# Optimization experiments

Measured on AMD Instinct MI355X. Metric: run time of the kernel, lower is better.

The kernel has to match this reference:

```python
import jax, jax.numpy as jnp
import numpy as np

S, B, D = 2048, 2, 768
H = 12
R = 64  # adapter bottleneck


def setup_inputs() -> dict:
    key = jax.random.key(0)
    ks = jax.random.split(key, 16)
    d = {
        'query': jax.random.normal(ks[0], (S, B, D), jnp.float32),
        'key':   jax.random.normal(ks[1], (S, B, D), jnp.float32),
        'value': jax.random.normal(ks[2], (S, B, D), jnp.float32),
        'in_proj_w': jax.random.normal(ks[3], (3 * D, D), jnp.float32) * (D ** -0.5),
        'in_proj_b': jax.random.normal(ks[4], (3 * D,), jnp.float32) * 0.02,
        'ssf_scale_1': 1.0 + 0.02 * jax.random.normal(ks[5], (3 * D,), jnp.float32),
        'ssf_shift_1': 0.02 * jax.random.normal(ks[6], (3 * D,), jnp.float32),
        'lora1_down_w': jax.random.normal(ks[7], (R, D), jnp.float32) * (D ** -0.5),
        'lora1_down_b': jnp.zeros((R,), jnp.float32),
        'lora1_up_w': jax.random.normal(ks[8], (3 * D, R), jnp.float32) * 0.02,
        'lora1_up_b': jnp.zeros((3 * D,), jnp.float32),
        'lora1_scale': jnp.ones((1,), jnp.float32),
        'out_w': jax.random.normal(ks[9], (D, D), jnp.float32) * (D ** -0.5),
        'out_b': jnp.zeros((D,), jnp.float32),
        'ssf_scale_2': 1.0 + 0.02 * jax.random.normal(ks[10], (D,), jnp.float32),
        'ssf_shift_2': 0.02 * jax.random.normal(ks[11], (D,), jnp.float32),
        'lora2_down_w': jax.random.normal(ks[12], (R, D), jnp.float32) * (D ** -0.5),
        'lora2_down_b': jnp.zeros((R,), jnp.float32),
        'lora2_up_w': jax.random.normal(ks[13], (D, R), jnp.float32) * 0.02,
        'lora2_up_b': jnp.zeros((D,), jnp.float32),
        'lora2_scale': jnp.ones((1,), jnp.float32),
        'num_heads': H,
    }
    return d


def _adapter(x, dw, db, uw, ub, scale):
    # down -> relu -> up -> * scalar (dropout inactive, add_residual=False)
    h = jax.nn.relu(jnp.einsum('sbd,rd->sbr', x, dw) + db)
    return (jnp.einsum('sbr,er->sbe', h, uw) + ub) * scale[0]


def reference(query, key, value, in_proj_w, in_proj_b, ssf_scale_1, ssf_shift_1,
              lora1_down_w, lora1_down_b, lora1_up_w, lora1_up_b, lora1_scale,
              out_w, out_b, ssf_scale_2, ssf_shift_2,
              lora2_down_w, lora2_down_b, lora2_up_w, lora2_up_b, lora2_scale,
              num_heads):
    tgt, bsz, d = query.shape
    hd = d // num_heads
    scaling = hd ** -0.5
    # fused QKV projection + SSF scale/shift + LoRA adapter on query
    qkv = jnp.einsum('sbd,ed->sbe', query, in_proj_w) + in_proj_b
    qkv = qkv * ssf_scale_1 + ssf_shift_1
    qkv = qkv + _adapter(query, lora1_down_w, lora1_down_b, lora1_up_w, lora1_up_b, lora1_scale)
    q, k, v = jnp.split(qkv, 3, axis=-1)
    q = q * scaling
    # [S,B,D] -> [B*H, S, hd]
    def to_heads(t):
        return t.reshape(tgt, bsz * num_heads, hd).transpose(1, 0, 2)
    q, k, v = to_heads(q), to_heads(k), to_heads(v)
    attn = jax.nn.softmax(jnp.einsum('nqh,nkh->nqk', q, k), axis=-1)
    out = jnp.einsum('nqk,nkh->nqh', attn, v)  # [B*H, S, hd]
    out = out.transpose(1, 0, 2).reshape(tgt, bsz, d)
    # lora2 on pre-projection attn output
    ad2 = _adapter(out, lora2_down_w, lora2_down_b, lora2_up_w, lora2_up_b, lora2_scale)
    o = jnp.einsum('sbd,ed->sbe', out, out_w) + out_b
    o = o * ssf_scale_2 + ssf_shift_2
    return o + ad2
```

## Files before the change

### kernel.cpp

```cpp
#include <hip/hip_runtime.h>
#include <stdint.h>

typedef float f32x4 __attribute__((ext_vector_type(4)));
typedef _Float16 f16x8 __attribute__((ext_vector_type(8)));
typedef _Float16 f16x4 __attribute__((ext_vector_type(4)));
typedef unsigned int u32x2 __attribute__((ext_vector_type(2)));

#define MFMAH(a, b, c) __builtin_amdgcn_mfma_f32_16x16x32_f16(a, b, c, 0, 0, 0)

#define GLOAD16(gp, lp) __builtin_amdgcn_global_load_lds( \
    (__attribute__((address_space(1))) void*)(void*)(gp), \
    (__attribute__((address_space(3))) void*)(void*)(lp), 16, 0, 0)

#define QSCALE (0.125f * 1.44269504f)
#define SMOFF 8.0f

static __device__ inline f32x4 zero4() { f32x4 z; z[0]=0.f; z[1]=0.f; z[2]=0.f; z[3]=0.f; return z; }

static __device__ inline unsigned int pk2(float a, float b) {
  return __builtin_bit_cast(unsigned int, __builtin_amdgcn_cvt_pkrtz(a, b));
}

__global__ void k_tof16_multi(const float* __restrict__ s0, const float* __restrict__ s1,
                              const float* __restrict__ s2, const float* __restrict__ s3,
                              const float* __restrict__ s4,
                              _Float16* __restrict__ d0, _Float16* __restrict__ d1,
                              _Float16* __restrict__ d2, _Float16* __restrict__ d3,
                              _Float16* __restrict__ d4,
                              int n0, int n1, int n2, int n3, int n4) {
  int total = n0 + n1 + n2 + n3 + n4;
  for (int i = blockIdx.x*blockDim.x + threadIdx.x; i < total; i += gridDim.x*blockDim.x) {
    const float* src; _Float16* dst; int j = i;
    if (j < n0) { src = s0; dst = d0; }
    else { j -= n0;
      if (j < n1) { src = s1; dst = d1; }
      else { j -= n1;
        if (j < n2) { src = s2; dst = d2; }
        else { j -= n2;
          if (j < n3) { src = s3; dst = d3; }
          else { j -= n3; src = s4; dst = d4; }
        }
      }
    }
    float4 v = ((const float4*)src)[j];
    f16x4 o;
    o[0] = (_Float16)v.x; o[1] = (_Float16)v.y; o[2] = (_Float16)v.z; o[3] = (_Float16)v.w;
    ((f16x4*)dst)[j] = o;
  }
}

__global__ void k_prep(const float* __restrict__ uw1, const float* __restrict__ s1,
                       const float* __restrict__ lsc1, _Float16* __restrict__ up1,
                       const float* __restrict__ uw2, const float* __restrict__ s2,
                       const float* __restrict__ lsc2, _Float16* __restrict__ up2,
                       const float* __restrict__ b1, const float* __restrict__ sh1,
                       const float* __restrict__ ub1, float* __restrict__ c1,
                       const float* __restrict__ b2, const float* __restrict__ sh2,
                       const float* __restrict__ ub2, float* __restrict__ c2) {
  int i = blockIdx.x*blockDim.x + threadIdx.x;
  if (i < 2304*64) up1[i] = (_Float16)(uw1[i] * lsc1[0] / s1[i >> 6]);
  if (i < 768*64)  up2[i] = (_Float16)(uw2[i] * lsc2[0] / s2[i >> 6]);
  if (i < 2304)    c1[i] = s1[i]*b1[i] + sh1[i] + lsc1[0]*ub1[i];
  if (i < 768)     c2[i] = s2[i]*b2[i] + sh2[i] + lsc2[0]*ub2[i];
}

__global__ __launch_bounds__(256) void k_lora_h(const _Float16* __restrict__ A,
    const _Float16* __restrict__ Dw, const float* __restrict__ db, _Float16* __restrict__ H) {
  const int wave = threadIdx.x >> 6, lane = threadIdx.x & 63;
  const int g = lane >> 4, li = lane & 15;
  const int rowbase = blockIdx.x * 16;
  f32x4 acc = zero4();
  for (int k0 = 0; k0 < 768; k0 += 32) {
    f16x8 a = *(const f16x8*)(A + (size_t)(rowbase + li)*768 + k0 + g*8);
    f16x8 b = *(const f16x8*)(Dw + (size_t)(wave*16 + li)*768 + k0 + g*8);
    acc = MFMAH(a, b, acc);
  }
  int r = wave*16 + li;
  float bias = db[r];
  #pragma unroll
  for (int j = 0; j < 4; j++) {
    float v = acc[j] + bias;
    H[(size_t)(rowbase + g*4 + j)*64 + r] = (_Float16)fmaxf(v, 0.f);
  }
}

template<int EPI>
__global__ __launch_bounds__(256) void k_gemm(
    const _Float16* __restrict__ A, const _Float16* __restrict__ B,
    const _Float16* __restrict__ Ha, const _Float16* __restrict__ Up,
    const float* __restrict__ Sc, const float* __restrict__ Cst,
    float* __restrict__ Cout, _Float16* __restrict__ qh,
    _Float16* __restrict__ kh, _Float16* __restrict__ vT) {
  __shared__ _Float16 lsA[2][4096];
  __shared__ _Float16 lsB[2][4096];
  const int wave = threadIdx.x >> 6, lane = threadIdx.x & 63;
  const int g = lane >> 4, li = lane & 15;
  const int wr = wave >> 1, wc = wave & 1;
  const int rb = blockIdx.x * 128, cb = blockIdx.y * 128;

  f32x4 acc[4][4];
  #pragma unroll
  for (int m = 0; m < 4; m++)
    #pragma unroll
    for (int n = 0; n < 4; n++) acc[m][n] = zero4();

  auto stage = [&](int buf, int k0) {
    #pragma unroll
    for (int c = 0; c < 2; c++) {
      int p = (wave*2 + c)*64 + lane;
      int r = p >> 2, cp = p & 3;
      int cc = (cp - (r >> 1)) & 3;
      GLOAD16(A + (size_t)(rb + r)*768 + k0 + cc*8, &lsA[buf][(wave*2 + c)*512]);
      GLOAD16(B + (size_t)(cb + r)*768 + k0 + cc*8, &lsB[buf][(wave*2 + c)*512]);
    }
  };

  stage(0, 0);
  __syncthreads();
  int cur = 0;
  for (int t = 0; t < 24; t++) {
    if (t + 1 < 24) stage(cur ^ 1, (t + 1) * 32);
    f16x8 ah[4], bh[4];
    #pragma unroll
    for (int m = 0; m < 4; m++) {
      int row = wr*64 + m*16 + li;
      int cp = (g + (row >> 1)) & 3;
      ah[m] = *(const f16x8*)(&lsA[cur][row*32 + cp*8]);
    }
    #pragma unroll
    for (int n = 0; n < 4; n++) {
      int row = wc*64 + n*16 + li;
      int cp = (g + (row >> 1)) & 3;
      bh[n] = *(const f16x8*)(&lsB[cur][row*32 + cp*8]);
    }
    __builtin_amdgcn_s_setprio(1);
    #pragma unroll
    for (int m = 0; m < 4; m++)
      #pragma unroll
      for (int n = 0; n < 4; n++)
        acc[m][n] = MFMAH(ah[m], bh[n], acc[m][n]);
    __builtin_amdgcn_s_setprio(0);
    __syncthreads();
    cur ^= 1;
  }

  _Float16* l0a = &lsA[0][0];
  _Float16* l0b = &lsB[0][0];
  #pragma unroll
  for (int c = 0; c < 4; c++) {
    int p = (wave*4 + c)*64 + lane;
    int r = p >> 3, cp = p & 7;
    int cc = (cp - r) & 7;
    GLOAD16(Ha + (size_t)(rb + r)*64 + cc*8, l0a + (wave*4 + c)*512);
    GLOAD16(Up + (size_t)(cb + r)*64 + cc*8, l0b + (wave*4 + c)*512);
  }
  __syncthreads();
  #pragma unroll
  for (int s = 0; s < 2; s++) {
    f16x8 ha[4], ub[4];
    #pragma unroll
    for (int m = 0; m < 4; m++) {
      int row = wr*64 + m*16 + li;
      int cp = ((s*4 + g) + row) & 7;
      ha[m] = *(const f16x8*)(l0a + row*64 + cp*8);
    }
    #pragma unroll
    for (int n = 0; n < 4; n++) {
      int row = wc*64 + n*16 + li;
      int cp = ((s*4 + g) + row) & 7;
      ub[n] = *(const f16x8*)(l0b + row*64 + cp*8);
    }
    #pragma unroll
    for (int m = 0; m < 4; m++)
      #pragma unroll
      for (int n = 0; n < 4; n++)
        acc[m][n] = MFMAH(ha[m], ub[n], acc[m][n]);
  }

  #pragma unroll
  for (int n = 0; n < 4; n++) {
    int col = cb + wc*64 + n*16 + li;
    float sc = Sc[col], ct = Cst[col];
    #pragma unroll
    for (int m = 0; m < 4; m++) {
      #pragma unroll
      for (int j = 0; j < 4; j++) {
        int row = rb + wr*64 + m*16 + g*4 + j;
        float v = sc * acc[m][n][j] + ct;
        if (EPI == 0) {
          Cout[(size_t)row*768 + col] = v;
        } else {
          int sect = col / 768;
          int eh = col - sect*768;
          int hh = eh >> 6, hd = eh & 63;
          int si = row >> 1, bb = row & 1;
          int nh = bb*12 + hh;
          if (sect == 0)      qh[((size_t)nh*2048 + si)*64 + hd] = (_Float16)(v * QSCALE);
          else if (sect == 1) kh[((size_t)nh*2048 + si)*64 + hd] = (_Float16)v;
          else                vT[((size_t)nh*64 + hd)*2048 + si] = (_Float16)v;
        }
      }
    }
  }
}

__global__ __launch_bounds__(256) void k_attn(const _Float16* __restrict__ qh,
    const _Float16* __restrict__ kh, const _Float16* __restrict__ vT,
    _Float16* __restrict__ outf) {
  const int wave = threadIdx.x >> 6, lane = threadIdx.x & 63;
  const int g = lane >> 4, li = lane & 15;
  const int head = blockIdx.y;
  const int q0 = blockIdx.x*64 + wave*16;
  const _Float16* Qb = qh + (size_t)head*2048*64;
  const _Float16* Kb = kh + (size_t)head*2048*64;
  const _Float16* Vb = vT + (size_t)head*64*2048;
  __shared__ _Float16 Kt[2][4096];
  __shared__ _Float16 Vt[2][4096];
  __shared__ _Float16 Pl[4][16*72];
  _Float16* myP = &Pl[wave][0];

  auto stage = [&](int buf, int kb) {
    #pragma unroll
    for (int c = 0; c < 2; c++) {
      int idx = c*256 + wave*64 + lane;
      int r = idx >> 3, cp = idx & 7;
      int csrc = cp ^ (r & 7);
      GLOAD16(Kb + (size_t)(kb + r)*64 + csrc*8, &Kt[buf][(c*256 + wave*64)*8]);
      GLOAD16(Vb + (size_t)r*2048 + kb + csrc*8, &Vt[buf][(c*256 + wave*64)*8]);
    }
  };

  f16x8 qf0 = *(const f16x8*)(Qb + (size_t)(q0 + li)*64 + g*8);
  f16x8 qf1 = *(const f16x8*)(Qb + (size_t)(q0 + li)*64 + 32 + g*8);
  f16x8 ones;
  #pragma unroll
  for (int i = 0; i < 8; i++) ones[i] = (_Float16)1.0f;
  f32x4 o[4];
  #pragma unroll
  for (int d = 0; d < 4; d++) o[d] = zero4();
  f32x4 o_l = zero4();
  const int sw = li & 7;

  stage(0, 0);
  __syncthreads();
  int cur = 0;
  for (int t = 0; t < 32; t++) {
    if (t + 1 < 32) stage(cur ^ 1, (t + 1) * 64);
    const _Float16* Kl = &Kt[cur][0];
    const _Float16* Vl = &Vt[cur][0];
    f32x4 c[4];
    __builtin_amdgcn_s_setprio(1);
    #pragma unroll
    for (int t4 = 0; t4 < 4; t4++) {
      int r = 16*t4 + li;
      f16x8 kf0 = *(const f16x8*)(Kl + r*64 + (g ^ sw)*8);
      f16x8 kf1 = *(const f16x8*)(Kl + r*64 + ((g + 4) ^ sw)*8);
      c[t4][0] = -SMOFF; c[t4][1] = -SMOFF; c[t4][2] = -SMOFF; c[t4][3] = -SMOFF;
      c[t4] = MFMAH(kf0, qf0, c[t4]);
      c[t4] = MFMAH(kf1, qf1, c[t4]);
    }
    __builtin_amdgcn_s_setprio(0);
    #pragma unroll
    for (int t4 = 0; t4 < 4; t4++) {
      u32x2 pk;
      pk[0] = pk2(__builtin_amdgcn_exp2f(c[t4][0]), __builtin_amdgcn_exp2f(c[t4][1]));
      pk[1] = pk2(__builtin_amdgcn_exp2f(c[t4][2]), __builtin_amdgcn_exp2f(c[t4][3]));
      *(u32x2*)(&myP[li*72 + 16*t4 + 4*g]) = pk;
    }
    __builtin_amdgcn_s_setprio(1);
    #pragma unroll
    for (int ks = 0; ks < 2; ks++) {
      f16x8 pf = *(const f16x8*)(&myP[li*72 + ks*32 + g*8]);
      #pragma unroll
      for (int d = 0; d < 4; d++) {
        int vr = d*16 + li;
        f16x8 vf = *(const f16x8*)(Vl + vr*64 + ((ks*4 + g) ^ sw)*8);
        o[d] = MFMAH(vf, pf, o[d]);
      }
      o_l = MFMAH(ones, pf, o_l);
    }
    __builtin_amdgcn_s_setprio(0);
    __syncthreads();
    cur ^= 1;
  }
  float inv = 1.f / o_l[0];
  const int bb = head / 12, hh = head % 12;
  const int si = q0 + li;
  #pragma unroll
  for (int d = 0; d < 4; d++) {
    f16x4 ov;
    #pragma unroll
    for (int j = 0; j < 4; j++) ov[j] = (_Float16)(o[d][j] * inv);
    *(f16x4*)(&outf[((size_t)si*2 + bb)*768 + hh*64 + d*16 + 4*g]) = ov;
  }
}

extern "C" void kernel_launch(void* const* d_in, const int* in_sizes, int n_in,
                              void* d_out, int out_size, void* d_ws, size_t ws_size,
                              hipStream_t stream) {
  (void)in_sizes; (void)n_in; (void)out_size; (void)ws_size;
  const float* query = (const float*)d_in[0];
  const float* w1   = (const float*)d_in[3];
  const float* b1   = (const float*)d_in[4];
  const float* s1   = (const float*)d_in[5];
  const float* sh1  = (const float*)d_in[6];
  const float* dw1  = (const float*)d_in[7];
  const float* db1  = (const float*)d_in[8];
  const float* uw1  = (const float*)d_in[9];
  const float* ub1  = (const float*)d_in[10];
  const float* lsc1 = (const float*)d_in[11];
  const float* w2   = (const float*)d_in[12];
  const float* b2   = (const float*)d_in[13];
  const float* s2   = (const float*)d_in[14];
  const float* sh2  = (const float*)d_in[15];
  const float* dw2  = (const float*)d_in[16];
  const float* db2  = (const float*)d_in[17];
  const float* uw2  = (const float*)d_in[18];
  const float* ub2  = (const float*)d_in[19];
  const float* lsc2 = (const float*)d_in[20];
  float* out = (float*)d_out;

  char* ws = (char*)d_ws;
  size_t off = 0;
  auto alloc = [&](size_t bytes) -> char* {
    char* p = ws + off; off += (bytes + 255) & ~(size_t)255; return p;
  };
  typedef _Float16 F16;
  F16* qf16 = (F16*)alloc((size_t)4096*768*2);
  F16* w1f  = (F16*)alloc((size_t)2304*768*2);
  F16* w2f  = (F16*)alloc((size_t)768*768*2);
  F16* d1f  = (F16*)alloc((size_t)64*768*2);
  F16* d2f  = (F16*)alloc((size_t)64*768*2);
  F16* up1p = (F16*)alloc((size_t)2304*64*2);
  F16* up2p = (F16*)alloc((size_t)768*64*2);
  float* c1 = (float*)alloc((size_t)2304*4);
  float* c2 = (float*)alloc((size_t)768*4);
  F16* h1   = (F16*)alloc((size_t)4096*64*2);
  F16* h2   = (F16*)alloc((size_t)4096*64*2);
  F16* qhd  = (F16*)alloc((size_t)24*2048*64*2);
  F16* khd  = (F16*)alloc((size_t)24*2048*64*2);
  F16* vTd  = (F16*)alloc((size_t)24*64*2048*2);
  F16* of16 = (F16*)alloc((size_t)4096*768*2);

  k_tof16_multi<<<2048, 256, 0, stream>>>(query, w1, w2, dw1, dw2,
                                          qf16, w1f, w2f, d1f, d2f,
                                          4096*768/4, 2304*768/4, 768*768/4,
                                          64*768/4, 64*768/4);
  k_prep<<<576, 256, 0, stream>>>(uw1, s1, lsc1, up1p, uw2, s2, lsc2, up2p,
                                  b1, sh1, ub1, c1, b2, sh2, ub2, c2);
  k_lora_h<<<256, 256, 0, stream>>>(qf16, d1f, db1, h1);
  k_gemm<1><<<dim3(32, 18), 256, 0, stream>>>(qf16, w1f, h1, up1p, s1, c1,
                                              nullptr, qhd, khd, vTd);
  k_attn<<<dim3(32, 24), 256, 0, stream>>>(qhd, khd, vTd, of16);
  k_lora_h<<<256, 256, 0, stream>>>(of16, d2f, db2, h2);
  k_gemm<0><<<dim3(32, 6), 256, 0, stream>>>(of16, w2f, h2, up2p, s2, c2,
                                             out, nullptr, nullptr, nullptr);
}
```

Measured before the change: 123.6 us.

## Process two query tiles per wave in attention to reuse K/V fragments

The attention kernel now uses 2 waves per block instead of 4. Each wave handles 32 query rows as two 16-row tiles, so every K and V fragment read from LDS feeds two MFMAs. This cuts LDS read traffic per FLOP and raises MFMA density. In exchange each wave holds more accumulators and registers, a block has fewer waves to hide latency, and each wave issues twice as many global-to-LDS staging loads.

```diff
diff --git a/kernel.cpp b/kernel.cpp
--- a/kernel.cpp
+++ b/kernel.cpp
@@ -204,41 +204,48 @@
   }
 }
 
-__global__ __launch_bounds__(256) void k_attn(const _Float16* __restrict__ qh,
+__global__ __launch_bounds__(128) void k_attn(const _Float16* __restrict__ qh,
     const _Float16* __restrict__ kh, const _Float16* __restrict__ vT,
     _Float16* __restrict__ outf) {
   const int wave = threadIdx.x >> 6, lane = threadIdx.x & 63;
   const int g = lane >> 4, li = lane & 15;
   const int head = blockIdx.y;
-  const int q0 = blockIdx.x*64 + wave*16;
+  const int q0 = blockIdx.x*64 + wave*32;
   const _Float16* Qb = qh + (size_t)head*2048*64;
   const _Float16* Kb = kh + (size_t)head*2048*64;
   const _Float16* Vb = vT + (size_t)head*64*2048;
   __shared__ _Float16 Kt[2][4096];
   __shared__ _Float16 Vt[2][4096];
-  __shared__ _Float16 Pl[4][16*72];
+  __shared__ _Float16 Pl[2][32*72];
   _Float16* myP = &Pl[wave][0];
 
   auto stage = [&](int buf, int kb) {
     #pragma unroll
-    for (int c = 0; c < 2; c++) {
-      int idx = c*256 + wave*64 + lane;
+    for (int c = 0; c < 4; c++) {
+      int idx = c*128 + wave*64 + lane;
       int r = idx >> 3, cp = idx & 7;
       int csrc = cp ^ (r & 7);
-      GLOAD16(Kb + (size_t)(kb + r)*64 + csrc*8, &Kt[buf][(c*256 + wave*64)*8]);
-      GLOAD16(Vb + (size_t)r*2048 + kb + csrc*8, &Vt[buf][(c*256 + wave*64)*8]);
+      GLOAD16(Kb + (size_t)(kb + r)*64 + csrc*8, &Kt[buf][(c*128 + wave*64)*8]);
+      GLOAD16(Vb + (size_t)r*2048 + kb + csrc*8, &Vt[buf][(c*128 + wave*64)*8]);
     }
   };
 
-  f16x8 qf0 = *(const f16x8*)(Qb + (size_t)(q0 + li)*64 + g*8);
-  f16x8 qf1 = *(const f16x8*)(Qb + (size_t)(q0 + li)*64 + 32 + g*8);
+  f16x8 qf[2][2];
+  #pragma unroll
+  for (int qt = 0; qt < 2; qt++) {
+    qf[qt][0] = *(const f16x8*)(Qb + (size_t)(q0 + qt*16 + li)*64 + g*8);
+    qf[qt][1] = *(const f16x8*)(Qb + (size_t)(q0 + qt*16 + li)*64 + 32 + g*8);
+  }
   f16x8 ones;
   #pragma unroll
   for (int i = 0; i < 8; i++) ones[i] = (_Float16)1.0f;
-  f32x4 o[4];
-  #pragma unroll
-  for (int d = 0; d < 4; d++) o[d] = zero4();
-  f32x4 o_l = zero4();
+  f32x4 o[4][2];
+  #pragma unroll
+  for (int d = 0; d < 4; d++)
+    #pragma unroll
+    for (int qt = 0; qt < 2; qt++) o[d][qt] = zero4();
+  f32x4 o_l[2];
+  o_l[0] = zero4(); o_l[1] = zero4();
   const int sw = li & 7;
 
   stage(0, 0);
@@ -248,50 +255,66 @@
     if (t + 1 < 32) stage(cur ^ 1, (t + 1) * 64);
     const _Float16* Kl = &Kt[cur][0];
     const _Float16* Vl = &Vt[cur][0];
-    f32x4 c[4];
+    f32x4 c[2][4];
     __builtin_amdgcn_s_setprio(1);
     #pragma unroll
     for (int t4 = 0; t4 < 4; t4++) {
       int r = 16*t4 + li;
       f16x8 kf0 = *(const f16x8*)(Kl + r*64 + (g ^ sw)*8);
       f16x8 kf1 = *(const f16x8*)(Kl + r*64 + ((g + 4) ^ sw)*8);
-      c[t4][0] = -SMOFF; c[t4][1] = -SMOFF; c[t4][2] = -SMOFF; c[t4][3] = -SMOFF;
-      c[t4] = MFMAH(kf0, qf0, c[t4]);
-      c[t4] = MFMAH(kf1, qf1, c[t4]);
+      #pragma unroll
+      for (int qt = 0; qt < 2; qt++) {
+        c[qt][t4][0] = -SMOFF; c[qt][t4][1] = -SMOFF;
+        c[qt][t4][2] = -SMOFF; c[qt][t4][3] = -SMOFF;
+        c[qt][t4] = MFMAH(kf0, qf[qt][0], c[qt][t4]);
+        c[qt][t4] = MFMAH(kf1, qf[qt][1], c[qt][t4]);
+      }
     }
     __builtin_amdgcn_s_setprio(0);
     #pragma unroll
-    for (int t4 = 0; t4 < 4; t4++) {
-      u32x2 pk;
-      pk[0] = pk2(__builtin_amdgcn_exp2f(c[t4][0]), __builtin_amdgcn_exp2f(c[t4][1]));
-      pk[1] = pk2(__builtin_amdgcn_exp2f(c[t4][2]), __builtin_amdgcn_exp2f(c[t4][3]));
-      *(u32x2*)(&myP[li*72 + 16*t4 + 4*g]) = pk;
-    }
+    for (int qt = 0; qt < 2; qt++)
+      #pragma unroll
+      for (int t4 = 0; t4 < 4; t4++) {
+        u32x2 pk;
+        pk[0] = pk2(__builtin_amdgcn_exp2f(c[qt][t4][0]), __builtin_amdgcn_exp2f(c[qt][t4][1]));
+        pk[1] = pk2(__builtin_amdgcn_exp2f(c[qt][t4][2]), __builtin_amdgcn_exp2f(c[qt][t4][3]));
+        *(u32x2*)(&myP[(qt*16 + li)*72 + 16*t4 + 4*g]) = pk;
+      }
     __builtin_amdgcn_s_setprio(1);
     #pragma unroll
     for (int ks = 0; ks < 2; ks++) {
-      f16x8 pf = *(const f16x8*)(&myP[li*72 + ks*32 + g*8]);
+      f16x8 pf[2];
+      #pragma unroll
+      for (int qt = 0; qt < 2; qt++)
+        pf[qt] = *(const f16x8*)(&myP[(qt*16 + li)*72 + ks*32 + g*8]);
       #pragma unroll
       for (int d = 0; d < 4; d++) {
         int vr = d*16 + li;
         f16x8 vf = *(const f16x8*)(Vl + vr*64 + ((ks*4 + g) ^ sw)*8);
-        o[d] = MFMAH(vf, pf, o[d]);
-      }
-      o_l = MFMAH(ones, pf, o_l);
+        #pragma unroll
+        for (int qt = 0; qt < 2; qt++)
+          o[d][qt] = MFMAH(vf, pf[qt], o[d][qt]);
+      }
+      #pragma unroll
+      for (int qt = 0; qt < 2; qt++)
+        o_l[qt] = MFMAH(ones, pf[qt], o_l[qt]);
     }
     __builtin_amdgcn_s_setprio(0);
     __syncthreads();
     cur ^= 1;
   }
-  float inv = 1.f / o_l[0];
   const int bb = head / 12, hh = head % 12;
-  const int si = q0 + li;
-  #pragma unroll
-  for (int d = 0; d < 4; d++) {
-    f16x4 ov;
-    #pragma unroll
-    for (int j = 0; j < 4; j++) ov[j] = (_Float16)(o[d][j] * inv);
-    *(f16x4*)(&outf[((size_t)si*2 + bb)*768 + hh*64 + d*16 + 4*g]) = ov;
+  #pragma unroll
+  for (int qt = 0; qt < 2; qt++) {
+    float inv = 1.f / o_l[qt][0];
+    const int si = q0 + qt*16 + li;
+    #pragma unroll
+    for (int d = 0; d < 4; d++) {
+      f16x4 ov;
+      #pragma unroll
+      for (int j = 0; j < 4; j++) ov[j] = (_Float16)(o[d][qt][j] * inv);
+      *(f16x4*)(&outf[((size_t)si*2 + bb)*768 + hh*64 + d*16 + 4*g]) = ov;
+    }
   }
 }
 
@@ -351,7 +374,7 @@
   k_lora_h<<<256, 256, 0, stream>>>(qf16, d1f, db1, h1);
   k_gemm<1><<<dim3(32, 18), 256, 0, stream>>>(qf16, w1f, h1, up1p, s1, c1,
                                               nullptr, qhd, khd, vTd);
-  k_attn<<<dim3(32, 24), 256, 0, stream>>>(qhd, khd, vTd, of16);
+  k_attn<<<dim3(32, 24), 128, 0, stream>>>(qhd, khd, vTd, of16);
   k_lora_h<<<256, 256, 0, stream>>>(of16, d2f, db2, h2);
   k_gemm<0><<<dim3(32, 6), 256, 0, stream>>>(of16, w2f, h2, up2p, s2, c2,
                                              out, nullptr, nullptr, nullptr);
```

Result: slower. 130.1 us (+5.3%).

## Deepen attention K/V prefetch to a 4-buffer ring with counted vmcnt waits

Applied to the files above, without the earlier changes.

Replaces the double-buffered K/V LDS staging in the attention kernel with a four-slot ring that keeps three tiles in flight. The full __syncthreads after each iteration becomes a single s_barrier per iteration, gated by explicit s_waitcnt vmcnt counts. Source addresses are also precomputed outside the loop so each stage issues four direct-to-LDS loads. The aim is to hide global load latency behind more MFMA work. In exchange it doubles the K/V LDS footprint, which can lower occupancy, and relies on hand-counted vmcnt values whose correctness depends on no other vector memory ops being outstanding.

```diff
diff --git a/kernel.cpp b/kernel.cpp
--- a/kernel.cpp
+++ b/kernel.cpp
@@ -214,24 +214,31 @@
   const _Float16* Qb = qh + (size_t)head*2048*64;
   const _Float16* Kb = kh + (size_t)head*2048*64;
   const _Float16* Vb = vT + (size_t)head*64*2048;
-  __shared__ _Float16 Kt[2][4096];
-  __shared__ _Float16 Vt[2][4096];
+  __shared__ _Float16 Kt[4][4096];
+  __shared__ _Float16 Vt[4][4096];
   __shared__ _Float16 Pl[4][16*72];
   _Float16* myP = &Pl[wave][0];
 
+  const int idx0 = wave*64 + lane, idx1 = 256 + wave*64 + lane;
+  const int r0 = idx0 >> 3, cs0 = (idx0 & 7) ^ (r0 & 7);
+  const int r1 = idx1 >> 3, cs1 = (idx1 & 7) ^ (r1 & 7);
+  const _Float16* srcK0 = Kb + (size_t)r0*64 + cs0*8;
+  const _Float16* srcK1 = Kb + (size_t)r1*64 + cs1*8;
+  const _Float16* srcV0 = Vb + (size_t)r0*2048 + cs0*8;
+  const _Float16* srcV1 = Vb + (size_t)r1*2048 + cs1*8;
+
   auto stage = [&](int buf, int kb) {
-    #pragma unroll
-    for (int c = 0; c < 2; c++) {
-      int idx = c*256 + wave*64 + lane;
-      int r = idx >> 3, cp = idx & 7;
-      int csrc = cp ^ (r & 7);
-      GLOAD16(Kb + (size_t)(kb + r)*64 + csrc*8, &Kt[buf][(c*256 + wave*64)*8]);
-      GLOAD16(Vb + (size_t)r*2048 + kb + csrc*8, &Vt[buf][(c*256 + wave*64)*8]);
-    }
+    GLOAD16(srcK0 + (size_t)kb*64, &Kt[buf][wave*512]);
+    GLOAD16(srcK1 + (size_t)kb*64, &Kt[buf][2048 + wave*512]);
+    GLOAD16(srcV0 + kb, &Vt[buf][wave*512]);
+    GLOAD16(srcV1 + kb, &Vt[buf][2048 + wave*512]);
   };
 
   f16x8 qf0 = *(const f16x8*)(Qb + (size_t)(q0 + li)*64 + g*8);
   f16x8 qf1 = *(const f16x8*)(Qb + (size_t)(q0 + li)*64 + 32 + g*8);
+  asm volatile("s_waitcnt vmcnt(0)" ::: "memory");
+  asm volatile("" : "+v"(qf0), "+v"(qf1));
+
   f16x8 ones;
   #pragma unroll
   for (int i = 0; i < 8; i++) ones[i] = (_Float16)1.0f;
@@ -242,12 +249,17 @@
   const int sw = li & 7;
 
   stage(0, 0);
-  __syncthreads();
-  int cur = 0;
+  stage(1, 64);
+  stage(2, 128);
   for (int t = 0; t < 32; t++) {
-    if (t + 1 < 32) stage(cur ^ 1, (t + 1) * 64);
-    const _Float16* Kl = &Kt[cur][0];
-    const _Float16* Vl = &Vt[cur][0];
+    if (t <= 29)      asm volatile("s_waitcnt vmcnt(8)" ::: "memory");
+    else if (t == 30) asm volatile("s_waitcnt vmcnt(4)" ::: "memory");
+    else              asm volatile("s_waitcnt vmcnt(0)" ::: "memory");
+    __builtin_amdgcn_s_barrier();
+    __builtin_amdgcn_sched_barrier(0);
+    if (t + 3 < 32) stage((t + 3) & 3, (t + 3) * 64);
+    const _Float16* Kl = &Kt[t & 3][0];
+    const _Float16* Vl = &Vt[t & 3][0];
     f32x4 c[4];
     __builtin_amdgcn_s_setprio(1);
     #pragma unroll
@@ -280,8 +292,6 @@
       o_l = MFMAH(ones, pf, o_l);
     }
     __builtin_amdgcn_s_setprio(0);
-    __syncthreads();
-    cur ^= 1;
   }
   float inv = 1.f / o_l[0];
   const int bb = head / 12, hh = head % 12;
```

Measured after the change: 147.2 us. 19.1% more time.

## Split attention key tile across waves and keep probabilities in registers

Applied to the files above, without the earlier changes.

Each wave in the attention kernel now handles 16 keys of every 64-key tile for all 64 queries, instead of owning 16 query rows. This lets the exponentiated scores feed the P·V MFMA (now the 16x16x16 variant) straight from registers, with no LDS round-trip for P. Row sums are accumulated with scalar adds instead of a ones-vector MFMA. The price is a cross-wave reduction at the end: partial outputs are stored to shared memory in fp16 and summed, which costs some precision. The change also uses a denser register footprint and sets launch bounds for three blocks per CU.

```diff
diff --git a/kernel.cpp b/kernel.cpp
--- a/kernel.cpp
+++ b/kernel.cpp
@@ -6,7 +6,8 @@
 typedef _Float16 f16x4 __attribute__((ext_vector_type(4)));
 typedef unsigned int u32x2 __attribute__((ext_vector_type(2)));
 
-#define MFMAH(a, b, c) __builtin_amdgcn_mfma_f32_16x16x32_f16(a, b, c, 0, 0, 0)
+#define MFMAH(a, b, c)  __builtin_amdgcn_mfma_f32_16x16x32_f16(a, b, c, 0, 0, 0)
+#define MFMAH16(a, b, c) __builtin_amdgcn_mfma_f32_16x16x16f16(a, b, c, 0, 0, 0)
 
 #define GLOAD16(gp, lp) __builtin_amdgcn_global_load_lds( \
     (__attribute__((address_space(1))) void*)(void*)(gp), \
@@ -204,20 +205,19 @@
   }
 }
 
-__global__ __launch_bounds__(256) void k_attn(const _Float16* __restrict__ qh,
+__global__ __launch_bounds__(256, 3) void k_attn(const _Float16* __restrict__ qh,
     const _Float16* __restrict__ kh, const _Float16* __restrict__ vT,
     _Float16* __restrict__ outf) {
   const int wave = threadIdx.x >> 6, lane = threadIdx.x & 63;
   const int g = lane >> 4, li = lane & 15;
   const int head = blockIdx.y;
-  const int q0 = blockIdx.x*64 + wave*16;
+  const int q0 = blockIdx.x*64;
   const _Float16* Qb = qh + (size_t)head*2048*64;
   const _Float16* Kb = kh + (size_t)head*2048*64;
   const _Float16* Vb = vT + (size_t)head*64*2048;
-  __shared__ _Float16 Kt[2][4096];
-  __shared__ _Float16 Vt[2][4096];
-  __shared__ _Float16 Pl[4][16*72];
-  _Float16* myP = &Pl[wave][0];
+  __shared__ char smem[36864];
+  _Float16* Kt = (_Float16*)smem;
+  _Float16* Vt = (_Float16*)(smem + 16384);
 
   auto stage = [&](int buf, int kb) {
     #pragma unroll
@@ -225,20 +225,24 @@
       int idx = c*256 + wave*64 + lane;
       int r = idx >> 3, cp = idx & 7;
       int csrc = cp ^ (r & 7);
-      GLOAD16(Kb + (size_t)(kb + r)*64 + csrc*8, &Kt[buf][(c*256 + wave*64)*8]);
-      GLOAD16(Vb + (size_t)r*2048 + kb + csrc*8, &Vt[buf][(c*256 + wave*64)*8]);
+      GLOAD16(Kb + (size_t)(kb + r)*64 + csrc*8, Kt + buf*4096 + (c*256 + wave*64)*8);
+      GLOAD16(Vb + (size_t)r*2048 + kb + csrc*8, Vt + buf*4096 + (c*256 + wave*64)*8);
     }
   };
 
-  f16x8 qf0 = *(const f16x8*)(Qb + (size_t)(q0 + li)*64 + g*8);
-  f16x8 qf1 = *(const f16x8*)(Qb + (size_t)(q0 + li)*64 + 32 + g*8);
-  f16x8 ones;
-  #pragma unroll
-  for (int i = 0; i < 8; i++) ones[i] = (_Float16)1.0f;
-  f32x4 o[4];
-  #pragma unroll
-  for (int d = 0; d < 4; d++) o[d] = zero4();
-  f32x4 o_l = zero4();
+  f16x8 qf[4][2];
+  #pragma unroll
+  for (int ct = 0; ct < 4; ct++)
+    #pragma unroll
+    for (int dw = 0; dw < 2; dw++)
+      qf[ct][dw] = *(const f16x8*)(Qb + (size_t)(q0 + 16*ct + li)*64 + dw*32 + g*8);
+
+  f32x4 o[4][4];
+  #pragma unroll
+  for (int dt = 0; dt < 4; dt++)
+    #pragma unroll
+    for (int qt = 0; qt < 4; qt++) o[dt][qt] = zero4();
+  float sj[4] = {0.f, 0.f, 0.f, 0.f};
   const int sw = li & 7;
 
   stage(0, 0);
@@ -246,52 +250,82 @@
   int cur = 0;
   for (int t = 0; t < 32; t++) {
     if (t + 1 < 32) stage(cur ^ 1, (t + 1) * 64);
-    const _Float16* Kl = &Kt[cur][0];
-    const _Float16* Vl = &Vt[cur][0];
+    const _Float16* Kl = Kt + cur*4096;
+    const _Float16* Vl = Vt + cur*4096;
+    const int krow = 16*wave + li;
+    f16x8 kf0 = *(const f16x8*)(Kl + krow*64 + (g ^ sw)*8);
+    f16x8 kf1 = *(const f16x8*)(Kl + krow*64 + ((4 + g) ^ sw)*8);
     f32x4 c[4];
     __builtin_amdgcn_s_setprio(1);
     #pragma unroll
-    for (int t4 = 0; t4 < 4; t4++) {
-      int r = 16*t4 + li;
-      f16x8 kf0 = *(const f16x8*)(Kl + r*64 + (g ^ sw)*8);
-      f16x8 kf1 = *(const f16x8*)(Kl + r*64 + ((g + 4) ^ sw)*8);
-      c[t4][0] = -SMOFF; c[t4][1] = -SMOFF; c[t4][2] = -SMOFF; c[t4][3] = -SMOFF;
-      c[t4] = MFMAH(kf0, qf0, c[t4]);
-      c[t4] = MFMAH(kf1, qf1, c[t4]);
+    for (int ct = 0; ct < 4; ct++) {
+      c[ct][0] = -SMOFF; c[ct][1] = -SMOFF; c[ct][2] = -SMOFF; c[ct][3] = -SMOFF;
+      c[ct] = MFMAH(kf0, qf[ct][0], c[ct]);
+      c[ct] = MFMAH(kf1, qf[ct][1], c[ct]);
     }
     __builtin_amdgcn_s_setprio(0);
-    #pragma unroll
-    for (int t4 = 0; t4 < 4; t4++) {
-      u32x2 pk;
-      pk[0] = pk2(__builtin_amdgcn_exp2f(c[t4][0]), __builtin_amdgcn_exp2f(c[t4][1]));
-      pk[1] = pk2(__builtin_amdgcn_exp2f(c[t4][2]), __builtin_amdgcn_exp2f(c[t4][3]));
-      *(u32x2*)(&myP[li*72 + 16*t4 + 4*g]) = pk;
+    f16x4 pf[4];
+    #pragma unroll
+    for (int ct = 0; ct < 4; ct++) {
+      float p0 = __builtin_amdgcn_exp2f(c[ct][0]);
+      float p1 = __builtin_amdgcn_exp2f(c[ct][1]);
+      float p2 = __builtin_amdgcn_exp2f(c[ct][2]);
+      float p3 = __builtin_amdgcn_exp2f(c[ct][3]);
+      sj[ct] += (p0 + p1) + (p2 + p3);
+      u32x2 pk; pk[0] = pk2(p0, p1); pk[1] = pk2(p2, p3);
+      pf[ct] = __builtin_bit_cast(f16x4, pk);
     }
     __builtin_amdgcn_s_setprio(1);
     #pragma unroll
-    for (int ks = 0; ks < 2; ks++) {
-      f16x8 pf = *(const f16x8*)(&myP[li*72 + ks*32 + g*8]);
+    for (int dt = 0; dt < 4; dt++) {
+      const int drow = 16*dt + li;
+      const _Float16* va = Vl + drow*64 + (((2*wave + (g >> 1)) ^ sw)*8) + 4*(g & 1);
+      f16x4 vf = *(const f16x4*)va;
       #pragma unroll
-      for (int d = 0; d < 4; d++) {
-        int vr = d*16 + li;
-        f16x8 vf = *(const f16x8*)(Vl + vr*64 + ((ks*4 + g) ^ sw)*8);
-        o[d] = MFMAH(vf, pf, o[d]);
-      }
-      o_l = MFMAH(ones, pf, o_l);
+      for (int qt = 0; qt < 4; qt++)
+        o[dt][qt] = MFMAH16(vf, pf[qt], o[dt][qt]);
     }
     __builtin_amdgcn_s_setprio(0);
     __syncthreads();
     cur ^= 1;
   }
-  float inv = 1.f / o_l[0];
+
+  _Float16* part = (_Float16*)smem;
+  float* lrp = (float*)(smem + 32768);
+  #pragma unroll
+  for (int dt = 0; dt < 4; dt++)
+    #pragma unroll
+    for (int qt = 0; qt < 4; qt++) {
+      u32x2 pw;
+      pw[0] = pk2(o[dt][qt][0], o[dt][qt][1]);
+      pw[1] = pk2(o[dt][qt][2], o[dt][qt][3]);
+      *(u32x2*)(part + ((wave*16 + dt*4 + qt)*64 + lane)*4) = pw;
+    }
+  #pragma unroll
+  for (int ct = 0; ct < 4; ct++) {
+    float a = sj[ct];
+    a += __shfl_xor(a, 16);
+    a += __shfl_xor(a, 32);
+    lrp[(wave*4 + ct)*64 + lane] = a;
+  }
+  __syncthreads();
   const int bb = head / 12, hh = head % 12;
-  const int si = q0 + li;
-  #pragma unroll
-  for (int d = 0; d < 4; d++) {
+  #pragma unroll
+  for (int qt = 0; qt < 4; qt++) {
+    float lr = lrp[qt*64 + lane] + lrp[(4 + qt)*64 + lane]
+             + lrp[(8 + qt)*64 + lane] + lrp[(12 + qt)*64 + lane];
+    float inv = 1.f / lr;
+    float s0 = 0.f, s1 = 0.f, s2 = 0.f, s3 = 0.f;
+    #pragma unroll
+    for (int p = 0; p < 4; p++) {
+      f16x4 pv = *(const f16x4*)(part + ((p*16 + wave*4 + qt)*64 + lane)*4);
+      s0 += (float)pv[0]; s1 += (float)pv[1]; s2 += (float)pv[2]; s3 += (float)pv[3];
+    }
+    const int si = q0 + 16*qt + li;
     f16x4 ov;
-    #pragma unroll
-    for (int j = 0; j < 4; j++) ov[j] = (_Float16)(o[d][j] * inv);
-    *(f16x4*)(&outf[((size_t)si*2 + bb)*768 + hh*64 + d*16 + 4*g]) = ov;
+    ov[0] = (_Float16)(s0 * inv); ov[1] = (_Float16)(s1 * inv);
+    ov[2] = (_Float16)(s2 * inv); ov[3] = (_Float16)(s3 * inv);
+    *(f16x4*)(&outf[((size_t)si*2 + bb)*768 + hh*64 + 16*wave + 4*g]) = ov;
   }
 }
 
```

Result: faster. 117.9 us (-4.6%).
